# Kernel tuning notes

Hardware: AMD Instinct MI355X
Metric: run time of the kernel (lower is better)

## Reference

```python
import jax, jax.numpy as jnp
import numpy as np

MAX_LEN = 128

def _lstm_cell(x, h, c, Wih, Whh, b):
    # PyTorch LSTM gate order: i, f, g, o ; b = b_ih + b_hh folded together
    gates = x @ Wih.T + h @ Whh.T + b
    i, f, g, o = jnp.split(gates, 4, axis=-1)
    c = jax.nn.sigmoid(f) * c + jax.nn.sigmoid(i) * jnp.tanh(g)
    h = jax.nn.sigmoid(o) * jnp.tanh(c)
    return h, c

def _lstm_scan(xs, h0, c0, Wih, Whh, b):
    # xs: [S, B, D_in] -> ys: [S, B, H], final (h, c)
    def step(carry, x):
        h, c = _lstm_cell(x, carry[0], carry[1], Wih, Whh, b)
        return (h, c), h
    (h, c), ys = jax.lax.scan(step, (h0, c0), xs)
    return ys, h, c

def setup_inputs():
    key = jax.random.key(0)
    B, S, E, H, VIN, VOUT = 32, 128, 256, 256, 32000, 16000
    Hd = 2 * H  # decoder hidden (bidirectional encoder states concatenated)
    ki = iter(jax.random.split(key, 32))
    def p(shape, scale):
        return jax.random.normal(next(ki), shape, dtype=jnp.float32) * scale
    s = 1.0 / float(np.sqrt(H))
    sd = 1.0 / float(np.sqrt(Hd))
    d = {}
    d['inputs'] = jax.random.randint(next(ki), (B, S), 0, VIN, dtype=jnp.int32)
    d['cls_token'] = 1
    d['in_emb'] = p((VIN, E), 0.02)
    d['out_emb'] = p((VOUT, E), 0.02)
    # encoder layer 0 (in=E), layer 1 (in=2H), fwd/bwd directions
    d['enc0f_Wih'] = p((4 * H, E), s); d['enc0f_Whh'] = p((4 * H, H), s); d['enc0f_b'] = p((4 * H,), s)
    d['enc0b_Wih'] = p((4 * H, E), s); d['enc0b_Whh'] = p((4 * H, H), s); d['enc0b_b'] = p((4 * H,), s)
    d['enc1f_Wih'] = p((4 * H, 2 * H), s); d['enc1f_Whh'] = p((4 * H, H), s); d['enc1f_b'] = p((4 * H,), s)
    d['enc1b_Wih'] = p((4 * H, 2 * H), s); d['enc1b_Whh'] = p((4 * H, H), s); d['enc1b_b'] = p((4 * H,), s)
    # decoder: 2 layers, hidden Hd=2H, layer0 in=E, layer1 in=Hd
    d['dec0_Wih'] = p((4 * Hd, E), sd); d['dec0_Whh'] = p((4 * Hd, Hd), sd); d['dec0_b'] = p((4 * Hd,), sd)
    d['dec1_Wih'] = p((4 * Hd, Hd), sd); d['dec1_Whh'] = p((4 * Hd, Hd), sd); d['dec1_b'] = p((4 * Hd,), sd)
    d['linW'] = p((VOUT, Hd), sd); d['linb'] = p((VOUT,), sd)
    return d

def reference(inputs, cls_token, in_emb, out_emb,
              enc0f_Wih, enc0f_Whh, enc0f_b, enc0b_Wih, enc0b_Whh, enc0b_b,
              enc1f_Wih, enc1f_Whh, enc1f_b, enc1b_Wih, enc1b_Whh, enc1b_b,
              dec0_Wih, dec0_Whh, dec0_b, dec1_Wih, dec1_Whh, dec1_b,
              linW, linb):
    B = inputs.shape[0]
    H = enc0f_Whh.shape[1]
    V = linW.shape[0]
    z = jnp.zeros((B, H), dtype=in_emb.dtype)
    xs = in_emb[inputs].transpose(1, 0, 2)  # [S, B, E]
    # --- bidirectional 2-layer encoder ---
    yf, hf0, cf0 = _lstm_scan(xs, z, z, enc0f_Wih, enc0f_Whh, enc0f_b)
    yb, hb0, cb0 = _lstm_scan(xs[::-1], z, z, enc0b_Wih, enc0b_Whh, enc0b_b)
    xs1 = jnp.concatenate([yf, yb[::-1]], axis=-1)  # [S, B, 2H]
    _, hf1, cf1 = _lstm_scan(xs1, z, z, enc1f_Wih, enc1f_Whh, enc1f_b)
    _, hb1, cb1 = _lstm_scan(xs1[::-1], z, z, enc1b_Wih, enc1b_Whh, enc1b_b)
    # decoder init: concat fwd/bwd final states per layer (matches reshape/permute in torch code)
    h0 = jnp.concatenate([hf0, hb0], -1); c0 = jnp.concatenate([cf0, cb0], -1)
    h1 = jnp.concatenate([hf1, hb1], -1); c1 = jnp.concatenate([cf1, cb1], -1)
    tok0 = jnp.full((B,), cls_token, dtype=jnp.int32)
    def dec_step(carry, _):
        h0, c0, h1, c1, tok = carry
        xe = out_emb[tok]  # [B, E]
        h0, c0 = _lstm_cell(xe, h0, c0, dec0_Wih, dec0_Whh, dec0_b)
        h1, c1 = _lstm_cell(h0, h1, c1, dec1_Wih, dec1_Whh, dec1_b)
        pred = h1 @ linW.T + linb  # [B, V]
        tok = jnp.argmax(pred, axis=-1).astype(jnp.int32)
        return (h0, c0, h1, c1, tok), pred
    _, preds = jax.lax.scan(dec_step, (h0, c0, h1, c1, tok0), None, length=MAX_LEN - 1)
    first = jax.nn.one_hot(tok0, V, dtype=preds.dtype)[:, None, :]  # [B, 1, V]
    return jnp.concatenate([first, preds.transpose(1, 0, 2)], axis=1)  # [B, MAX_LEN, V]
```

## Files before the change

### kernel.cpp

```cpp
#include <hip/hip_runtime.h>

typedef unsigned long long u64;
typedef unsigned int u32;

#define Bz 32
#define Sz 128
#define Ez 256
#define Hz 256
#define Vz 16000
#define Tz 128

#define OFF_PART 8192u
#define OFF_HS   524288u
#define OUT_XS   0u
#define OUT_XS1  (4u<<20)

#define HS_H0A 98304
#define HS_H0B 114688
#define HS_C0  131072
#define HS_H1A 147456
#define HS_H1B 163840
#define HS_C1  180224
#define HS_N   196608

__device__ inline float sigf(float x){ return 1.0f/(1.0f+expf(-x)); }
__device__ inline u32 f2ord(float f){ u32 u=__float_as_uint(f); return (u & 0x80000000u) ? ~u : (u | 0x80000000u); }

#define ACC4(w, xp) { acc=fmaf((w).x,(xp)[0],acc); acc=fmaf((w).y,(xp)[1],acc); \
                      acc=fmaf((w).z,(xp)[2],acc); acc=fmaf((w).w,(xp)[3],acc); }

struct BarSlot { u32 cnt; u32 gen; };

__device__ inline void block_bar(BarSlot* s, u32 nblk, u32 target){
  __syncthreads();
  if (threadIdx.x == 0){
    u32 old = __hip_atomic_fetch_add(&s->cnt, 1u, __ATOMIC_ACQ_REL, __HIP_MEMORY_SCOPE_AGENT);
    if (old == nblk-1u){
      __hip_atomic_store(&s->cnt, 0u, __ATOMIC_RELAXED, __HIP_MEMORY_SCOPE_AGENT);
      __hip_atomic_fetch_add(&s->gen, 1u, __ATOMIC_RELEASE, __HIP_MEMORY_SCOPE_AGENT);
    } else {
      while (__hip_atomic_load(&s->gen, __ATOMIC_ACQUIRE, __HIP_MEMORY_SCOPE_AGENT) < target){
        __builtin_amdgcn_s_sleep(2);
      }
    }
  }
  __syncthreads();
}

__device__ inline u64 shfl_down_u64(u64 x, int d){
  int lo = __shfl_down((int)(u32)(x & 0xFFFFFFFFull), d, 64);
  int hi = __shfl_down((int)(u32)(x >> 32), d, 64);
  return (((u64)(u32)hi)<<32) | (u64)(u32)lo;
}

__global__ __launch_bounds__(256) void k_init(const int* __restrict__ inp,
    const float* __restrict__ iemb, char* __restrict__ outc, char* __restrict__ ws)
{
  float4* XS4 = (float4*)(outc + OUT_XS);
  const float4* IE4 = (const float4*)iemb;
  float4* HS4 = (float4*)(ws + OFF_HS);
  u64* PART = (u64*)(ws + OFF_PART);
  const int N1 = 262144;
  const int N2 = HS_N/4;
  const int N3 = 32768;
  const int TOT = N1+N2+N3;
  for (int i = blockIdx.x*256 + threadIdx.x; i < TOT; i += gridDim.x*256){
    int r = i;
    if (r < N1){
      int e4 = r & 63, sb = r >> 6;
      int b2 = sb & 31, s2 = sb >> 5;
      XS4[r] = IE4[(size_t)inp[b2*Sz + s2]*64 + e4];
    } else if ((r -= N1) < N2){
      HS4[r] = make_float4(0.f,0.f,0.f,0.f);
    } else {
      PART[r - N2] = 0ull;
    }
  }
}

__global__ __launch_bounds__(256) void k_enc(
    const float* __restrict__ Wfi, const float* __restrict__ Wfh, const float* __restrict__ bfv,
    const float* __restrict__ Wbi, const float* __restrict__ Wbh, const float* __restrict__ bbv,
    char* __restrict__ outc, char* __restrict__ ws, int layer)
{
  __shared__ __align__(16) float xh[1024];
  float* glds = xh + 768;
  int tid = threadIdx.x;
  int chain = blockIdx.x >> 7, c = blockIdx.x & 127;
  int b = c & 31, q = c >> 5, j0 = q*64;
  int g = tid >> 6, jj = tid & 63;
  int xK = layer ? 512 : 256;
  const float* X    = (const float*)(outc + (layer ? OUT_XS1 : OUT_XS));
  float*       XS1w = (float*)(outc + OUT_XS1);
  float* HSf = (float*)(ws + OFF_HS);
  float* chbase = HSf + layer*49152 + chain*24576;
  float* cst = chbase + 16384;
  const float* Wih  = chain ? Wbi : Wfi;
  const float* Whh  = chain ? Wbh : Wfh;
  const float* bias = chain ? bbv : bfv;
  int row = g*256 + j0 + jj;
  float bv = bias[row];
  BarSlot* bar = (BarSlot*)ws + (layer ? 64 : 0) + chain*32 + b;
  int dh_off = layer ? HS_H1A : HS_H0A;
  int dc_off = layer ? HS_C1  : HS_C0;
  const float4* wa  = (const float4*)(Wih + (size_t)row*xK);
  const float4* wb2 = (const float4*)(Whh + (size_t)row*256);

  for (int s = 0; s < 128; ++s){
    int xi = chain ? (127 - s) : s;
    const float* hbuf = chbase + (s&1)*8192;
    const float* xrow = X + ((size_t)xi*32 + b)*xK;
    xh[tid] = xrow[tid];
    if (layer) xh[256 + tid] = xrow[256 + tid];
    xh[xK + tid] = hbuf[b*256 + tid];
    __syncthreads();
    float acc = bv;
    int nA4 = xK >> 2;
    #pragma unroll 16
    for (int k4 = 0; k4 < nA4; ++k4){ float4 w = wa[k4]; ACC4(w, xh + (k4<<2)); }
    #pragma unroll 16
    for (int k4 = 0; k4 < 64; ++k4){ float4 w = wb2[k4]; ACC4(w, xh + xK + (k4<<2)); }
    glds[tid] = acc;
    __syncthreads();
    if (tid < 64){
      int j = j0 + tid;
      float iv = sigf(glds[tid]), fv = sigf(glds[64+tid]);
      float gv = tanhf(glds[128+tid]), ov = sigf(glds[192+tid]);
      float cold = cst[b*256 + j];
      float cnew = fv*cold + iv*gv;
      cst[b*256 + j] = cnew;
      float hnew = ov*tanhf(cnew);
      (chbase + ((s+1)&1)*8192)[b*256 + j] = hnew;
      if (layer == 0) XS1w[((size_t)xi*32 + b)*512 + chain*256 + j] = hnew;
      if (s == 127){
        HSf[dh_off + b*512 + chain*256 + j] = hnew;
        HSf[dc_off + b*512 + chain*256 + j] = cnew;
      }
    }
    if (s < 127) block_bar(bar, 4, (u32)(s+1));
  }
}

__global__ __launch_bounds__(256) void k_dec(const float* __restrict__ oemb,
    const float* __restrict__ W0i, const float* __restrict__ W0h, const float* __restrict__ b0v,
    const float* __restrict__ W1i, const float* __restrict__ W1h, const float* __restrict__ b1v,
    const float* __restrict__ linW, const float* __restrict__ linbv, const int* __restrict__ clsp,
    float* __restrict__ out, char* __restrict__ ws)
{
  __shared__ __align__(16) float smem[16384];
  float* xh   = smem;
  float* glds = smem + 1024;
  float* h1s  = smem;
  u64*  tokred = (u64*)(smem + 1024);

  int tid = threadIdx.x, blk = blockIdx.x;
  int b = (blk & 7) | ((blk >> 6) << 3), jgrp = (blk >> 3) & 7, j0 = jgrp*64;
  int g = tid >> 6, jj = tid & 63;
  int rowA = g*512 + j0 + jj;
  int vl = tid >> 5, bb = tid & 31, wv = tid >> 6, lane = tid & 63;
  int v0 = blk * 64;

  float* HSf = (float*)(ws + OFF_HS);
  u64* PART = (u64*)(ws + OFF_PART);
  BarSlot* bars = (BarSlot*)ws;
  BarSlot* bar_b = bars + 128 + b;
  BarSlot* bar_f = bars + 192;
  float bA = b0v[rowA];
  float bB = b1v[rowA];
  int cls = *clsp;
  u32 tgt_b = 0, tgt_f = 0;
  const float4* wA1 = (const float4*)(W0i + (size_t)rowA*256);
  const float4* wA2 = (const float4*)(W0h + (size_t)rowA*512);
  const float4* wB1 = (const float4*)(W1i + (size_t)rowA*512);
  const float4* wB2 = (const float4*)(W1h + (size_t)rowA*512);

  for (int step = 0; step < 127; ++step){
    int p = step & 1;
    float* h0r = HSf + (p ? HS_H0B : HS_H0A);
    float* h0w = HSf + (p ? HS_H0A : HS_H0B);
    float* h1r = HSf + (p ? HS_H1B : HS_H1A);
    float* h1w = HSf + (p ? HS_H1A : HS_H1B);

    int t_b;
    if (step == 0){ t_b = cls; }
    else {
      u64 pk = 0;
      for (int r = tid; r < 1000; r += 256){ u64 q2 = PART[(size_t)b*1024 + r]; if (q2 > pk) pk = q2; }
      #pragma unroll
      for (int d = 32; d; d >>= 1){ u64 o = shfl_down_u64(pk, d); if (o > pk) pk = o; }
      if (lane == 0) tokred[wv] = pk;
      __syncthreads();
      if (tid == 0){
        u64 m = tokred[0];
        for (int w2 = 1; w2 < 4; ++w2) if (tokred[w2] > m) m = tokred[w2];
        u32 tk = 0xFFFFFFFFu - (u32)(m & 0xFFFFFFFFull);
        if (tk >= (u32)Vz) tk = 0;
        xh[1023] = __uint_as_float(tk);
      }
      __syncthreads();
      t_b = (int)__float_as_uint(xh[1023]);
    }

    xh[tid]       = oemb[(size_t)t_b*Ez + tid];
    xh[256 + tid] = h0r[b*512 + tid];
    xh[512 + tid] = h0r[b*512 + 256 + tid];
    __syncthreads();
    float acc = bA;
    #pragma unroll 16
    for (int k4 = 0; k4 < 64; ++k4){ float4 w = wA1[k4]; ACC4(w, xh + (k4<<2)); }
    #pragma unroll 16
    for (int k4 = 0; k4 < 128; ++k4){ float4 w = wA2[k4]; ACC4(w, xh + 256 + (k4<<2)); }
    glds[tid] = acc;
    __syncthreads();
    if (tid < 64){
      int j = j0 + tid;
      float iv = sigf(glds[tid]), fv = sigf(glds[64+tid]);
      float gv = tanhf(glds[128+tid]), ov = sigf(glds[192+tid]);
      float* c0 = HSf + HS_C0;
      float cold = c0[b*512 + j], cnew = fv*cold + iv*gv;
      c0[b*512 + j] = cnew;
      h0w[b*512 + j] = ov*tanhf(cnew);
    }
    block_bar(bar_b, 8, ++tgt_b);

    xh[tid]       = h0w[b*512 + tid];
    xh[256 + tid] = h0w[b*512 + 256 + tid];
    xh[512 + tid] = h1r[b*512 + tid];
    xh[768 + tid] = h1r[b*512 + 256 + tid];
    __syncthreads();
    acc = bB;
    #pragma unroll 16
    for (int k4 = 0; k4 < 128; ++k4){ float4 w = wB1[k4]; ACC4(w, xh + (k4<<2)); }
    #pragma unroll 16
    for (int k4 = 0; k4 < 128; ++k4){ float4 w = wB2[k4]; ACC4(w, xh + 512 + (k4<<2)); }
    glds[tid] = acc;
    __syncthreads();
    if (tid < 64){
      int j = j0 + tid;
      float iv = sigf(glds[tid]), fv = sigf(glds[64+tid]);
      float gv = tanhf(glds[128+tid]), ov = sigf(glds[192+tid]);
      float* c1 = HSf + HS_C1;
      float cold = c1[b*512 + j], cnew = fv*cold + iv*gv;
      c1[b*512 + j] = cnew;
      h1w[b*512 + j] = ov*tanhf(cnew);
    }
    block_bar(bar_f, 256, ++tgt_f);

    for (int i2 = tid; i2 < 16384; i2 += 256){
      int b2 = i2 >> 9, k2 = i2 & 511;
      h1s[(i2 & ~511) | ((k2 + 4*b2) & 511)] = h1w[i2];
    }
    __syncthreads();
    if (blk < 250){
      int v8 = v0 + (vl<<3);
      float a[8];
      #pragma unroll
      for (int t = 0; t < 8; ++t) a[t] = linbv[v8 + t];
      const float4* wc = (const float4*)(linW + (size_t)v8*512);
      const float* hrow = h1s + (bb<<9);
      for (int k4 = 0; k4 < 128; ++k4){
        float4 hx = *(const float4*)(hrow + (((k4<<2) + 4*bb) & 511));
        #pragma unroll
        for (int t = 0; t < 8; ++t){
          float4 w = wc[t*128 + k4];
          a[t]=fmaf(w.x,hx.x,a[t]); a[t]=fmaf(w.y,hx.y,a[t]);
          a[t]=fmaf(w.z,hx.z,a[t]); a[t]=fmaf(w.w,hx.w,a[t]);
        }
      }
      float* orow = out + ((size_t)bb*Tz + (size_t)(step+1))*Vz + v8;
      *(float4*)(orow)     = make_float4(a[0],a[1],a[2],a[3]);
      *(float4*)(orow + 4) = make_float4(a[4],a[5],a[6],a[7]);
      if (step == 0){
        float* zrow = out + (size_t)bb*Tz*Vz + v8;
        float f0[8];
        #pragma unroll
        for (int t = 0; t < 8; ++t) f0[t] = (v8 + t == cls) ? 1.f : 0.f;
        *(float4*)(zrow)     = make_float4(f0[0],f0[1],f0[2],f0[3]);
        *(float4*)(zrow + 4) = make_float4(f0[4],f0[5],f0[6],f0[7]);
      }
      u32 bk = f2ord(a[0]); u32 bvv = (u32)v8;
      #pragma unroll
      for (int t = 1; t < 8; ++t){ u32 k2 = f2ord(a[t]); if (k2 > bk){ bk = k2; bvv = (u32)(v8 + t); } }
      u64 pk = (((u64)bk)<<32) | (u64)(0xFFFFFFFFu - bvv);
      u64 o = shfl_down_u64(pk, 32); if (o > pk) pk = o;
      if (lane < 32) PART[(size_t)bb*1024 + blk*4 + wv] = pk;
    }
    if (step < 126) block_bar(bar_f, 256, ++tgt_f);
    else ++tgt_f;
  }
}

extern "C" void kernel_launch(void* const* d_in, const int* in_sizes, int n_in,
                              void* d_out, int out_size, void* d_ws, size_t ws_size,
                              hipStream_t stream) {
  const int* inputs = (const int*)d_in[0];
  const int* cls    = (const int*)d_in[1];
  const float* in_emb = (const float*)d_in[2];
  const float* out_emb= (const float*)d_in[3];
  const float* e0f_Wih=(const float*)d_in[4],  *e0f_Whh=(const float*)d_in[5],  *e0f_b=(const float*)d_in[6];
  const float* e0b_Wih=(const float*)d_in[7],  *e0b_Whh=(const float*)d_in[8],  *e0b_b=(const float*)d_in[9];
  const float* e1f_Wih=(const float*)d_in[10], *e1f_Whh=(const float*)d_in[11], *e1f_b=(const float*)d_in[12];
  const float* e1b_Wih=(const float*)d_in[13], *e1b_Whh=(const float*)d_in[14], *e1b_b=(const float*)d_in[15];
  const float* d0_Wih =(const float*)d_in[16], *d0_Whh =(const float*)d_in[17], *d0_b =(const float*)d_in[18];
  const float* d1_Wih =(const float*)d_in[19], *d1_Whh =(const float*)d_in[20], *d1_b =(const float*)d_in[21];
  const float* linW   =(const float*)d_in[22], *linb   =(const float*)d_in[23];
  float* out = (float*)d_out;
  char* outc = (char*)d_out;
  char* ws = (char*)d_ws;

  hipMemsetAsync(ws, 0, 4096, stream);
  k_init<<<1024, 256, 0, stream>>>(inputs, in_emb, outc, ws);
  k_enc<<<256, 256, 0, stream>>>(e0f_Wih, e0f_Whh, e0f_b, e0b_Wih, e0b_Whh, e0b_b, outc, ws, 0);
  k_enc<<<256, 256, 0, stream>>>(e1f_Wih, e1f_Whh, e1f_b, e1b_Wih, e1b_Whh, e1b_b, outc, ws, 1);
  k_dec<<<256, 256, 0, stream>>>(out_emb, d0_Wih, d0_Whh, d0_b, d1_Wih, d1_Whh, d1_b,
                                 linW, linb, cls, out, ws);
}
```

Baseline: 27.32 ms.

## Restructure decoder: 1024-thread blocks, batch-tiled LSTM cells, hierarchical grid barrier

The decoder kernel now runs 1024 threads per block. Only 128 blocks compute the LSTM cells, each handling 4 batch rows with the K dimension split across thread groups and reduced in shared memory, so each weight load is reused across 4 batch rows. The vocab projection gives each thread 2 outputs instead of 8, and the argmax partials are reduced in-block first so fewer entries go to global memory. A two-level grid barrier (8 sub-counters feeding a master counter) replaces the flat 256-block counter to reduce atomic contention. The encoder's block-to-(batch, quarter) mapping is also changed. The cost is a larger per-block footprint, heavier reliance on all 256 large blocks being co-resident, and an added LDS reduction step.

```diff
diff --git a/kernel.cpp b/kernel.cpp
--- a/kernel.cpp
+++ b/kernel.cpp
@@ -28,6 +28,12 @@
 
 #define ACC4(w, xp) { acc=fmaf((w).x,(xp)[0],acc); acc=fmaf((w).y,(xp)[1],acc); \
                       acc=fmaf((w).z,(xp)[2],acc); acc=fmaf((w).w,(xp)[3],acc); }
+
+#define ACC4X(w, p) { \
+  acc0=fmaf((w).x,(p)[0],acc0);    acc0=fmaf((w).y,(p)[1],acc0);    acc0=fmaf((w).z,(p)[2],acc0);    acc0=fmaf((w).w,(p)[3],acc0); \
+  acc1=fmaf((w).x,(p)[1024],acc1); acc1=fmaf((w).y,(p)[1025],acc1); acc1=fmaf((w).z,(p)[1026],acc1); acc1=fmaf((w).w,(p)[1027],acc1); \
+  acc2=fmaf((w).x,(p)[2048],acc2); acc2=fmaf((w).y,(p)[2049],acc2); acc2=fmaf((w).z,(p)[2050],acc2); acc2=fmaf((w).w,(p)[2051],acc2); \
+  acc3=fmaf((w).x,(p)[3072],acc3); acc3=fmaf((w).y,(p)[3073],acc3); acc3=fmaf((w).z,(p)[3074],acc3); acc3=fmaf((w).w,(p)[3075],acc3); }
 
 struct BarSlot { u32 cnt; u32 gen; };
 
@@ -40,6 +46,32 @@
       __hip_atomic_fetch_add(&s->gen, 1u, __ATOMIC_RELEASE, __HIP_MEMORY_SCOPE_AGENT);
     } else {
       while (__hip_atomic_load(&s->gen, __ATOMIC_ACQUIRE, __HIP_MEMORY_SCOPE_AGENT) < target){
+        __builtin_amdgcn_s_sleep(2);
+      }
+    }
+  }
+  __syncthreads();
+}
+
+__device__ inline void grid_bar(char* ws, u32 target){
+  __syncthreads();
+  if (threadIdx.x == 0){
+    u32* sub  = (u32*)(ws + 2048 + (size_t)(blockIdx.x & 7)*128);
+    u32* mcnt = (u32*)(ws + 3072);
+    u32* gen  = (u32*)(ws + 3200);
+    bool rel = false;
+    u32 old = __hip_atomic_fetch_add(sub, 1u, __ATOMIC_ACQ_REL, __HIP_MEMORY_SCOPE_AGENT);
+    if (old == 31u){
+      __hip_atomic_store(sub, 0u, __ATOMIC_RELAXED, __HIP_MEMORY_SCOPE_AGENT);
+      u32 mo = __hip_atomic_fetch_add(mcnt, 1u, __ATOMIC_ACQ_REL, __HIP_MEMORY_SCOPE_AGENT);
+      if (mo == 7u){
+        __hip_atomic_store(mcnt, 0u, __ATOMIC_RELAXED, __HIP_MEMORY_SCOPE_AGENT);
+        __hip_atomic_fetch_add(gen, 1u, __ATOMIC_RELEASE, __HIP_MEMORY_SCOPE_AGENT);
+        rel = true;
+      }
+    }
+    if (!rel){
+      while (__hip_atomic_load(gen, __ATOMIC_ACQUIRE, __HIP_MEMORY_SCOPE_AGENT) < target){
         __builtin_amdgcn_s_sleep(2);
       }
     }
@@ -87,7 +119,7 @@
   float* glds = xh + 768;
   int tid = threadIdx.x;
   int chain = blockIdx.x >> 7, c = blockIdx.x & 127;
-  int b = c & 31, q = c >> 5, j0 = q*64;
+  int q = c & 3, b = c >> 2, j0 = q*64;
   int g = tid >> 6, jj = tid & 63;
   int xK = layer ? 512 : 256;
   const float* X    = (const float*)(outc + (layer ? OUT_XS1 : OUT_XS));
@@ -141,7 +173,7 @@
   }
 }
 
-__global__ __launch_bounds__(256) void k_dec(const float* __restrict__ oemb,
+__global__ __launch_bounds__(1024) void k_dec(const float* __restrict__ oemb,
     const float* __restrict__ W0i, const float* __restrict__ W0h, const float* __restrict__ b0v,
     const float* __restrict__ W1i, const float* __restrict__ W1h, const float* __restrict__ b1v,
     const float* __restrict__ linW, const float* __restrict__ linbv, const int* __restrict__ clsp,
@@ -149,30 +181,45 @@
 {
   __shared__ __align__(16) float smem[16384];
   float* xh   = smem;
-  float* glds = smem + 1024;
+  float* glds = smem + 4096;
+  int*  stok  = (int*)(smem + 8192);
   float* h1s  = smem;
-  u64*  tokred = (u64*)(smem + 1024);
+  u64*  tokred = (u64*)smem;
 
   int tid = threadIdx.x, blk = blockIdx.x;
-  int b = (blk & 7) | ((blk >> 6) << 3), jgrp = (blk >> 3) & 7, j0 = jgrp*64;
-  int g = tid >> 6, jj = tid & 63;
-  int rowA = g*512 + j0 + jj;
-  int vl = tid >> 5, bb = tid & 31, wv = tid >> 6, lane = tid & 63;
+  int lane = tid & 63, wv = tid >> 6;
+
+  int jg = blk & 15, b4 = blk >> 4;
+  int kq = tid >> 7, r = tid & 127, g = r >> 5, jj = r & 31;
+  int rowA = g*512 + jg*32 + jj;
+
+  int vl = tid >> 5, bb = tid & 31;
   int v0 = blk * 64;
+  int v  = v0 + 2*vl;
+  int vsafe = (blk < 250) ? v : 0;
 
   float* HSf = (float*)(ws + OFF_HS);
   u64* PART = (u64*)(ws + OFF_PART);
-  BarSlot* bars = (BarSlot*)ws;
-  BarSlot* bar_b = bars + 128 + b;
-  BarSlot* bar_f = bars + 192;
-  float bA = b0v[rowA];
-  float bB = b1v[rowA];
+  BarSlot* bar_b = (BarSlot*)(ws + 1024 + (size_t)(b4 & 7)*128);
+  float* c0p = HSf + HS_C0;
+  float* c1p = HSf + HS_C1;
   int cls = *clsp;
   u32 tgt_b = 0, tgt_f = 0;
-  const float4* wA1 = (const float4*)(W0i + (size_t)rowA*256);
-  const float4* wA2 = (const float4*)(W0h + (size_t)rowA*512);
-  const float4* wB1 = (const float4*)(W1i + (size_t)rowA*512);
-  const float4* wB2 = (const float4*)(W1h + (size_t)rowA*512);
+  bool is_cell = (blk < 128);
+
+  float bAi=0,bAf=0,bAg=0,bAo=0,bBi=0,bBf=0,bBg=0,bBo=0;
+  if (tid < 128){
+    int jc = jg*32 + (tid & 31);
+    bAi=b0v[jc]; bAf=b0v[512+jc]; bAg=b0v[1024+jc]; bAo=b0v[1536+jc];
+    bBi=b1v[jc]; bBf=b1v[512+jc]; bBg=b1v[1024+jc]; bBo=b1v[1536+jc];
+  }
+  const float4* wA1 = (const float4*)(W0i + (size_t)rowA*256) + kq*8;
+  const float4* wA2 = (const float4*)(W0h + (size_t)rowA*512) + kq*16;
+  const float4* wB1 = (const float4*)(W1i + (size_t)rowA*512) + kq*16;
+  const float4* wB2 = (const float4*)(W1h + (size_t)rowA*512) + kq*16;
+  const float4* wc0 = (const float4*)(linW + (size_t)vsafe*512);
+  const float4* wc1 = wc0 + 128;
+  float lb0 = linbv[vsafe], lb1 = linbv[vsafe + 1];
 
   for (int step = 0; step < 127; ++step){
     int p = step & 1;
@@ -181,111 +228,146 @@
     float* h1r = HSf + (p ? HS_H1B : HS_H1A);
     float* h1w = HSf + (p ? HS_H1A : HS_H1B);
 
-    int t_b;
-    if (step == 0){ t_b = cls; }
-    else {
-      u64 pk = 0;
-      for (int r = tid; r < 1000; r += 256){ u64 q2 = PART[(size_t)b*1024 + r]; if (q2 > pk) pk = q2; }
-      #pragma unroll
-      for (int d = 32; d; d >>= 1){ u64 o = shfl_down_u64(pk, d); if (o > pk) pk = o; }
-      if (lane == 0) tokred[wv] = pk;
-      __syncthreads();
-      if (tid == 0){
-        u64 m = tokred[0];
-        for (int w2 = 1; w2 < 4; ++w2) if (tokred[w2] > m) m = tokred[w2];
-        u32 tk = 0xFFFFFFFFu - (u32)(m & 0xFFFFFFFFull);
-        if (tk >= (u32)Vz) tk = 0;
-        xh[1023] = __uint_as_float(tk);
-      }
-      __syncthreads();
-      t_b = (int)__float_as_uint(xh[1023]);
-    }
-
-    xh[tid]       = oemb[(size_t)t_b*Ez + tid];
-    xh[256 + tid] = h0r[b*512 + tid];
-    xh[512 + tid] = h0r[b*512 + 256 + tid];
-    __syncthreads();
-    float acc = bA;
-    #pragma unroll 16
-    for (int k4 = 0; k4 < 64; ++k4){ float4 w = wA1[k4]; ACC4(w, xh + (k4<<2)); }
-    #pragma unroll 16
-    for (int k4 = 0; k4 < 128; ++k4){ float4 w = wA2[k4]; ACC4(w, xh + 256 + (k4<<2)); }
-    glds[tid] = acc;
-    __syncthreads();
-    if (tid < 64){
-      int j = j0 + tid;
-      float iv = sigf(glds[tid]), fv = sigf(glds[64+tid]);
-      float gv = tanhf(glds[128+tid]), ov = sigf(glds[192+tid]);
-      float* c0 = HSf + HS_C0;
-      float cold = c0[b*512 + j], cnew = fv*cold + iv*gv;
-      c0[b*512 + j] = cnew;
-      h0w[b*512 + j] = ov*tanhf(cnew);
-    }
-    block_bar(bar_b, 8, ++tgt_b);
-
-    xh[tid]       = h0w[b*512 + tid];
-    xh[256 + tid] = h0w[b*512 + 256 + tid];
-    xh[512 + tid] = h1r[b*512 + tid];
-    xh[768 + tid] = h1r[b*512 + 256 + tid];
-    __syncthreads();
-    acc = bB;
-    #pragma unroll 16
-    for (int k4 = 0; k4 < 128; ++k4){ float4 w = wB1[k4]; ACC4(w, xh + (k4<<2)); }
-    #pragma unroll 16
-    for (int k4 = 0; k4 < 128; ++k4){ float4 w = wB2[k4]; ACC4(w, xh + 512 + (k4<<2)); }
-    glds[tid] = acc;
-    __syncthreads();
-    if (tid < 64){
-      int j = j0 + tid;
-      float iv = sigf(glds[tid]), fv = sigf(glds[64+tid]);
-      float gv = tanhf(glds[128+tid]), ov = sigf(glds[192+tid]);
-      float* c1 = HSf + HS_C1;
-      float cold = c1[b*512 + j], cnew = fv*cold + iv*gv;
-      c1[b*512 + j] = cnew;
-      h1w[b*512 + j] = ov*tanhf(cnew);
-    }
-    block_bar(bar_f, 256, ++tgt_f);
-
-    for (int i2 = tid; i2 < 16384; i2 += 256){
+    if (is_cell){
+      if (step == 0){
+        if (tid < 4) stok[tid] = cls;
+      } else if (wv < 4){
+        int bi = b4*4 + wv;
+        u64 pk = 0;
+        #pragma unroll
+        for (int q2 = 0; q2 < 4; ++q2){
+          int r2 = q2*64 + lane;
+          if (r2 < 250){ u64 e = PART[(size_t)bi*256 + r2]; if (e > pk) pk = e; }
+        }
+        #pragma unroll
+        for (int d = 32; d; d >>= 1){ u64 o = shfl_down_u64(pk, d); if (o > pk) pk = o; }
+        if (lane == 0){
+          u32 tk = 0xFFFFFFFFu - (u32)(pk & 0xFFFFFFFFull);
+          if (tk >= (u32)Vz) tk = 0;
+          stok[wv] = (int)tk;
+        }
+      }
+      __syncthreads();
+
+      {
+        int o = tid;
+        if (o < 256){
+          #pragma unroll
+          for (int i = 0; i < 4; ++i) xh[i*1024 + o] = oemb[(size_t)stok[i]*Ez + o];
+        } else if (o < 768){
+          #pragma unroll
+          for (int i = 0; i < 4; ++i) xh[i*1024 + o] = h0r[(size_t)(b4*4+i)*512 + (o-256)];
+        }
+      }
+      __syncthreads();
+      {
+        float acc0=0.f, acc1=0.f, acc2=0.f, acc3=0.f;
+        const float* xq = xh + kq*32;
+        const float* hq = xh + 256 + kq*64;
+        #pragma unroll
+        for (int k4 = 0; k4 < 8; ++k4){ float4 w = wA1[k4]; const float* p2 = xq + (k4<<2); ACC4X(w, p2); }
+        #pragma unroll 8
+        for (int k4 = 0; k4 < 16; ++k4){ float4 w = wA2[k4]; const float* p2 = hq + (k4<<2); ACC4X(w, p2); }
+        glds[tid] = acc0; glds[1024+tid] = acc1; glds[2048+tid] = acc2; glds[3072+tid] = acc3;
+      }
+      __syncthreads();
+      if (tid < 128){
+        int i = tid >> 5, jj2 = tid & 31;
+        int bi = b4*4 + i, j = jg*32 + jj2;
+        const float* gb = glds + i*1024;
+        float s0=0.f,s1=0.f,s2=0.f,s3=0.f;
+        #pragma unroll
+        for (int k2 = 0; k2 < 8; ++k2){
+          const float* gk = gb + k2*128;
+          s0 += gk[jj2]; s1 += gk[32+jj2]; s2 += gk[64+jj2]; s3 += gk[96+jj2];
+        }
+        float iv = sigf(s0 + bAi), fv = sigf(s1 + bAf);
+        float gv = tanhf(s2 + bAg), ov = sigf(s3 + bAo);
+        float cold = c0p[(size_t)bi*512 + j];
+        float cnew = fv*cold + iv*gv;
+        c0p[(size_t)bi*512 + j] = cnew;
+        h0w[(size_t)bi*512 + j] = ov*tanhf(cnew);
+      }
+      block_bar(bar_b, 16, ++tgt_b);
+
+      {
+        int o = tid;
+        if (o < 512){
+          #pragma unroll
+          for (int i = 0; i < 4; ++i) xh[i*1024 + o] = h0w[(size_t)(b4*4+i)*512 + o];
+        } else {
+          #pragma unroll
+          for (int i = 0; i < 4; ++i) xh[i*1024 + o] = h1r[(size_t)(b4*4+i)*512 + (o-512)];
+        }
+      }
+      __syncthreads();
+      {
+        float acc0=0.f, acc1=0.f, acc2=0.f, acc3=0.f;
+        const float* xq = xh + kq*64;
+        const float* hq = xh + 512 + kq*64;
+        #pragma unroll 8
+        for (int k4 = 0; k4 < 16; ++k4){ float4 w = wB1[k4]; const float* p2 = xq + (k4<<2); ACC4X(w, p2); }
+        #pragma unroll 8
+        for (int k4 = 0; k4 < 16; ++k4){ float4 w = wB2[k4]; const float* p2 = hq + (k4<<2); ACC4X(w, p2); }
+        glds[tid] = acc0; glds[1024+tid] = acc1; glds[2048+tid] = acc2; glds[3072+tid] = acc3;
+      }
+      __syncthreads();
+      if (tid < 128){
+        int i = tid >> 5, jj2 = tid & 31;
+        int bi = b4*4 + i, j = jg*32 + jj2;
+        const float* gb = glds + i*1024;
+        float s0=0.f,s1=0.f,s2=0.f,s3=0.f;
+        #pragma unroll
+        for (int k2 = 0; k2 < 8; ++k2){
+          const float* gk = gb + k2*128;
+          s0 += gk[jj2]; s1 += gk[32+jj2]; s2 += gk[64+jj2]; s3 += gk[96+jj2];
+        }
+        float iv = sigf(s0 + bBi), fv = sigf(s1 + bBf);
+        float gv = tanhf(s2 + bBg), ov = sigf(s3 + bBo);
+        float cold = c1p[(size_t)bi*512 + j];
+        float cnew = fv*cold + iv*gv;
+        c1p[(size_t)bi*512 + j] = cnew;
+        h1w[(size_t)bi*512 + j] = ov*tanhf(cnew);
+      }
+    }
+
+    grid_bar(ws, ++tgt_f);
+
+    for (int i2 = tid; i2 < 16384; i2 += 1024){
       int b2 = i2 >> 9, k2 = i2 & 511;
       h1s[(i2 & ~511) | ((k2 + 4*b2) & 511)] = h1w[i2];
     }
     __syncthreads();
     if (blk < 250){
-      int v8 = v0 + (vl<<3);
-      float a[8];
-      #pragma unroll
-      for (int t = 0; t < 8; ++t) a[t] = linbv[v8 + t];
-      const float4* wc = (const float4*)(linW + (size_t)v8*512);
-      const float* hrow = h1s + (bb<<9);
+      float a0 = lb0, a1 = lb1;
+      const float* hrow = h1s + (bb << 9);
+      #pragma unroll 4
       for (int k4 = 0; k4 < 128; ++k4){
         float4 hx = *(const float4*)(hrow + (((k4<<2) + 4*bb) & 511));
-        #pragma unroll
-        for (int t = 0; t < 8; ++t){
-          float4 w = wc[t*128 + k4];
-          a[t]=fmaf(w.x,hx.x,a[t]); a[t]=fmaf(w.y,hx.y,a[t]);
-          a[t]=fmaf(w.z,hx.z,a[t]); a[t]=fmaf(w.w,hx.w,a[t]);
-        }
-      }
-      float* orow = out + ((size_t)bb*Tz + (size_t)(step+1))*Vz + v8;
-      *(float4*)(orow)     = make_float4(a[0],a[1],a[2],a[3]);
-      *(float4*)(orow + 4) = make_float4(a[4],a[5],a[6],a[7]);
+        float4 w0 = wc0[k4], w1 = wc1[k4];
+        a0=fmaf(w0.x,hx.x,a0); a0=fmaf(w0.y,hx.y,a0); a0=fmaf(w0.z,hx.z,a0); a0=fmaf(w0.w,hx.w,a0);
+        a1=fmaf(w1.x,hx.x,a1); a1=fmaf(w1.y,hx.y,a1); a1=fmaf(w1.z,hx.z,a1); a1=fmaf(w1.w,hx.w,a1);
+      }
+      float* orow = out + ((size_t)bb*Tz + (size_t)(step+1))*Vz + v;
+      *(float2*)orow = make_float2(a0, a1);
       if (step == 0){
-        float* zrow = out + (size_t)bb*Tz*Vz + v8;
-        float f0[8];
-        #pragma unroll
-        for (int t = 0; t < 8; ++t) f0[t] = (v8 + t == cls) ? 1.f : 0.f;
-        *(float4*)(zrow)     = make_float4(f0[0],f0[1],f0[2],f0[3]);
-        *(float4*)(zrow + 4) = make_float4(f0[4],f0[5],f0[6],f0[7]);
-      }
-      u32 bk = f2ord(a[0]); u32 bvv = (u32)v8;
-      #pragma unroll
-      for (int t = 1; t < 8; ++t){ u32 k2 = f2ord(a[t]); if (k2 > bk){ bk = k2; bvv = (u32)(v8 + t); } }
+        float* zrow = out + (size_t)bb*Tz*Vz + v;
+        *(float2*)zrow = make_float2((v==cls)?1.f:0.f, (v+1==cls)?1.f:0.f);
+      }
+      u32 k0 = f2ord(a0), k1 = f2ord(a1);
+      u32 bk = k0; u32 bvv = (u32)v;
+      if (k1 > bk){ bk = k1; bvv = (u32)(v+1); }
       u64 pk = (((u64)bk)<<32) | (u64)(0xFFFFFFFFu - bvv);
-      u64 o = shfl_down_u64(pk, 32); if (o > pk) pk = o;
-      if (lane < 32) PART[(size_t)bb*1024 + blk*4 + wv] = pk;
-    }
-    if (step < 126) block_bar(bar_f, 256, ++tgt_f);
+      __syncthreads();
+      tokred[tid] = pk;
+      __syncthreads();
+      if (tid < 32){
+        u64 m = tokred[tid];
+        for (int q2 = 1; q2 < 32; ++q2){ u64 o = tokred[q2*32 + tid]; if (o > m) m = o; }
+        PART[(size_t)tid*256 + blk] = m;
+      }
+    }
+    if (step < 126) grid_bar(ws, ++tgt_f);
     else ++tgt_f;
   }
 }
@@ -312,6 +394,6 @@
   k_init<<<1024, 256, 0, stream>>>(inputs, in_emb, outc, ws);
   k_enc<<<256, 256, 0, stream>>>(e0f_Wih, e0f_Whh, e0f_b, e0b_Wih, e0b_Whh, e0b_b, outc, ws, 0);
   k_enc<<<256, 256, 0, stream>>>(e1f_Wih, e1f_Whh, e1f_b, e1b_Wih, e1b_Whh, e1b_b, outc, ws, 1);
-  k_dec<<<256, 256, 0, stream>>>(out_emb, d0_Wih, d0_Whh, d0_b, d1_Wih, d1_Whh, d1_b,
-                                 linW, linb, cls, out, ws);
-}
+  k_dec<<<256, 1024, 0, stream>>>(out_emb, d0_Wih, d0_Whh, d0_b, d1_Wih, d1_Whh, d1_b,
+                                  linW, linb, cls, out, ws);
+}
```

After: 38.93 ms. 42.5% more time.
